# Performance work log

Hardware: AMD Instinct MI355X
Metric: run time of the kernel (lower is better)

Reference implementation:

```python
import jax, jax.numpy as jnp
import numpy as np
from jax import lax

B, S, T = 32, 400, 100
V, OOV = 32000, 100
E, U, AU, GP, ENC = 512, 256, 256, 256, 512


def setup_inputs() -> dict:
    key = jax.random.key(0)
    ks = jax.random.split(key, 24)
    r = lambda k, shp: 0.02 * jax.random.normal(k, shp, dtype=jnp.float32)
    inp = {
        "gt_tokens": jax.random.randint(ks[0], (B, T), 0, V, dtype=jnp.int32),
        "extended_input_tokens": jax.random.randint(ks[1], (B, S), 0, V + OOV, dtype=jnp.int32),
        "enc_output": jax.random.normal(ks[2], (B, S, ENC), dtype=jnp.float32),
        "enc_attn": jax.random.normal(ks[3], (B, S, AU), dtype=jnp.float32),
        "h0": jnp.zeros((B, U), jnp.float32),
        "c0": jnp.zeros((B, U), jnp.float32),
        # learned parameters
        "emb": r(ks[4], (V, E)),
        "lstm_kernel": r(ks[5], (E, 4 * U)),
        "lstm_rec": r(ks[6], (U, 4 * U)),
        "lstm_bias": jnp.zeros((4 * U,), jnp.float32),
        "attn_Wd": r(ks[7], (2 * U, AU)),
        "attn_bd": jnp.zeros((AU,), jnp.float32),
        "attn_Wc": r(ks[8], (1, AU)),
        "attn_Wa": r(ks[9], (AU, 1)),
        "clf_W1": r(ks[10], (U, U)),
        "clf_b1": jnp.zeros((U,), jnp.float32),
        "clf_W2": r(ks[11], (U, V)),
        "clf_b2": jnp.zeros((V,), jnp.float32),
        "gp_Ws": r(ks[12], (2 * U, GP)),
        "gp_Wc": r(ks[13], (ENC, GP)),
        "gp_Wi": r(ks[14], (E, GP)),
        "gp_bi": jnp.zeros((GP,), jnp.float32),
        "gp_Wg": r(ks[15], (GP, 1)),
    }
    return inp


def _decode(gt_tokens, extended_input_tokens, enc_output, enc_attn, h0, c0,
            emb, lstm_kernel, lstm_rec, lstm_bias, attn_Wd, attn_bd, attn_Wc,
            attn_Wa, clf_W1, clf_b1, clf_W2, clf_b2, gp_Ws, gp_Wc, gp_Wi,
            gp_bi, gp_Wg):
    Bn, Sn = extended_input_tokens.shape
    gt_vec = emb[gt_tokens]                      # [B,T,E] teacher-forced inputs
    xs = jnp.swapaxes(gt_vec, 0, 1)              # [T,B,E]
    batch_idx = jnp.arange(Bn)[:, None]

    def step(carry, x):
        h, c, cov = carry                        # [B,U],[B,U],[B,S]
        # single-step LSTM (TF gate order i,f,g,o)
        z = x @ lstm_kernel + h @ lstm_rec + lstm_bias
        i_, f_, g_, o_ = jnp.split(z, 4, axis=-1)
        c = jax.nn.sigmoid(f_) * c + jax.nn.sigmoid(i_) * jnp.tanh(g_)
        h = jax.nn.sigmoid(o_) * jnp.tanh(c)
        dec_state = jnp.concatenate([h, c], axis=1)          # [B,2U]
        # Bahdanau attention with coverage
        dec_attn = dec_state @ attn_Wd + attn_bd             # [B,AU]
        cov_attn = cov[:, :, None] * attn_Wc[0]              # [B,S,AU]
        scores = jnp.tanh(enc_attn + cov_attn + dec_attn[:, None, :]) @ attn_Wa
        a = jax.nn.softmax(scores, axis=1)[:, :, 0]          # [B,S]
        c_vec = jnp.einsum('bse,bs->be', enc_output, a)      # [B,ENC]
        cov_loss = jnp.sum(jnp.minimum(cov, a), axis=1)      # [B]
        cov = cov + a
        # pg: faithful scalar quirk ([0,0,0] of broadcast sum in original)
        g = dec_state[0] @ gp_Ws + c_vec[0] @ gp_Wc + (x[0] @ gp_Wi + gp_bi)
        pg = jax.nn.sigmoid((g @ gp_Wg)[0])
        # vocab distribution, extended with OOV zeros
        vocab_p = jax.nn.softmax((h @ clf_W1 + clf_b1) @ clf_W2 + clf_b2, axis=-1)
        vocab_p = jnp.concatenate([vocab_p, jnp.zeros((Bn, OOV), vocab_p.dtype)], axis=1)
        # copy distribution via scatter-add of attention onto extended ids
        sent_p = jnp.zeros((Bn, V + OOV), a.dtype).at[batch_idx, extended_input_tokens].add(a)
        final = pg * vocab_p + (1.0 - pg) * sent_p           # [B,V+OOV]
        tok = jnp.argmax(final, axis=1).astype(jnp.int32)
        return (h, c, cov), (final, tok, cov_loss)

    cov0 = jnp.zeros((Bn, Sn), jnp.float32)
    _, (probs, seqs, cov_losses) = lax.scan(step, (h0, c0, cov0), xs)
    return (jnp.swapaxes(probs, 0, 1),       # [B,T,V+OOV]
            jnp.swapaxes(seqs, 0, 1),        # [B,T]
            jnp.swapaxes(cov_losses, 0, 1))  # [B,T]


def reference(gt_tokens, extended_input_tokens, enc_output, enc_attn, h0, c0,
              emb, lstm_kernel, lstm_rec, lstm_bias, attn_Wd, attn_bd,
              attn_Wc, attn_Wa, clf_W1, clf_b1, clf_W2, clf_b2, gp_Ws, gp_Wc,
              gp_Wi, gp_bi, gp_Wg):
    return _decode(gt_tokens, extended_input_tokens, enc_output, enc_attn, h0,
                   c0, emb, lstm_kernel, lstm_rec, lstm_bias, attn_Wd,
                   attn_bd, attn_Wc, attn_Wa, clf_W1, clf_b1, clf_W2, clf_b2,
                   gp_Ws, gp_Wc, gp_Wi, gp_bi, gp_Wg)
```

## Files before the change

kernel.cpp:

```cpp
#include <hip/hip_runtime.h>
#include <hip/hip_bf16.h>

#define Bn 32
#define Sn 400
#define Tn 100
#define Vn 32000
#define OOVn 100
#define VEn 32100
#define En 512
#define Un 256
#define AUn 256
#define GPn 256
#define ENCn 512
#define Z4n 1024

typedef __attribute__((ext_vector_type(8))) short bf16x8;
typedef __attribute__((ext_vector_type(4))) float f32x4;
typedef unsigned short ushort_t;
typedef unsigned long long u64;

__device__ __forceinline__ float rcp_f(float x){ return __builtin_amdgcn_rcpf(x); }
__device__ __forceinline__ float tanh_fast(float x){
  float e2 = __expf(2.f*x);
  return 1.f - 2.f*rcp_f(e2 + 1.f);
}
__device__ __forceinline__ float sigmoid_f(float x){ return 1.f/(1.f+__expf(-x)); }
__device__ __forceinline__ ushort_t f2bf(float f){
  unsigned u = __float_as_uint(f);
  unsigned r = (u + 0x7FFFu + ((u>>16)&1u)) >> 16;
  return (ushort_t)r;
}
__device__ __forceinline__ u64 shfl_xor_u64(u64 v, int m){
  unsigned lo = (unsigned)v, hi = (unsigned)(v>>32);
  lo = (unsigned)__shfl_xor((int)lo, m);
  hi = (unsigned)__shfl_xor((int)hi, m);
  return ((u64)hi<<32)|(u64)lo;
}

__device__ __forceinline__ void st_rlx(float* p, float v){
  __hip_atomic_store(p, v, __ATOMIC_RELAXED, __HIP_MEMORY_SCOPE_AGENT);
}
__device__ __forceinline__ float ld_rlx(const float* p){
  return __hip_atomic_load(p, __ATOMIC_RELAXED, __HIP_MEMORY_SCOPE_AGENT);
}
__device__ __forceinline__ void st_flag(unsigned* p, unsigned v){
  __hip_atomic_store(p, v, __ATOMIC_RELAXED, __HIP_MEMORY_SCOPE_AGENT);
}
__device__ __forceinline__ unsigned ld_flag(const unsigned* p){
  return __hip_atomic_load(p, __ATOMIC_RELAXED, __HIP_MEMORY_SCOPE_AGENT);
}


__global__ __launch_bounds__(256) void k_zx(const int* __restrict__ gt,
    const float* __restrict__ emb, const float* __restrict__ Wk,
    const float* __restrict__ bias, float* __restrict__ Zx,
    unsigned* __restrict__ bars, float* __restrict__ covloss){
  __shared__ float As[64][17];
  __shared__ float Bs[16][65];
  __shared__ int tok_lds[64];
  int r0 = blockIdx.x * 64;
  int c0 = blockIdx.y * 64;
  int tid = threadIdx.x;
  int ty = tid >> 4, tx = tid & 15;
  if (blockIdx.x == 0){
    int y = blockIdx.y;
    #pragma unroll
    for (int i = 0; i < 2; ++i){
      int idx = y*512 + i*256 + tid;
      bars[idx] = 0u;
    }
    if (tid < 200) covloss[y*200 + tid] = 0.f;
  }
  if (tid < 64){
    int r = r0 + tid;
    tok_lds[tid] = gt[(r & 31)*Tn + (r >> 5)];
  }
  __syncthreads();
  float acc[4][4] = {};
  for (int k0 = 0; k0 < En; k0 += 16){
    #pragma unroll
    for (int p = 0; p < 4; ++p){
      int row = (tid>>4) + p*16, kk = tid & 15;
      As[row][kk] = emb[(size_t)tok_lds[row]*En + k0 + kk];
    }
    #pragma unroll
    for (int p = 0; p < 4; ++p){
      int kk = (tid>>6) + p*4, cc = tid & 63;
      Bs[kk][cc] = Wk[(size_t)(k0+kk)*Z4n + c0 + cc];
    }
    __syncthreads();
    #pragma unroll
    for (int kk = 0; kk < 16; ++kk){
      float av[4], bv[4];
      #pragma unroll
      for (int i=0;i<4;++i) av[i] = As[ty*4+i][kk];
      #pragma unroll
      for (int j=0;j<4;++j) bv[j] = Bs[kk][tx*4+j];
      #pragma unroll
      for (int i=0;i<4;++i)
        #pragma unroll
        for (int j=0;j<4;++j) acc[i][j] += av[i]*bv[j];
    }
    __syncthreads();
  }
  #pragma unroll
  for (int i=0;i<4;++i){
    int row = r0 + ty*4 + i;
    #pragma unroll
    for (int j=0;j<4;++j){
      int col = c0 + tx*4 + j;
      Zx[(size_t)row*Z4n + col] = acc[i][j] + bias[col];
    }
  }
}


__global__ __launch_bounds__(1024, 1) void k_loop(
    const float* __restrict__ Zx, const float* __restrict__ Wr,
    const float* __restrict__ Wd, const float* __restrict__ bd,
    const float* __restrict__ Wc, const float* __restrict__ Wa,
    const float* __restrict__ enc_attn,
    const float* __restrict__ h0, const float* __restrict__ c0,
    float* __restrict__ h_all, float* __restrict__ decp,
    float* __restrict__ c0_all, float* __restrict__ a_all,
    float* __restrict__ covloss, float* __restrict__ spart,
    unsigned* __restrict__ bars){
  __shared__ float Wr_lds[256*128];
  __shared__ float hfull[Un];
  __shared__ float ppart[8][132];
  __shared__ float zx_lds[128];
  __shared__ float zfull[128];
  __shared__ float hnew[32], cown[32];
  __shared__ float dec_lds[AUn];
  __shared__ float cov_lds[50], sc_lds[50];
  __shared__ float wred[16];
  __shared__ float red8[8];

  const int b = blockIdx.x & 31, k = blockIdx.x >> 5;
  const int tid = threadIdx.x, lane = tid & 63, w = tid >> 6;
  unsigned* flags = bars + b*8*32;
  unsigned* myflag = flags + k*32;

  for (int idx = tid; idx < 256*128; idx += 1024){
    int u = idx >> 7, jl = idx & 127;
    int gcol = 32*k + (jl & 31) + 256*(jl >> 5);
    Wr_lds[idx] = Wr[(size_t)u*Z4n + gcol];
  }
  if (tid < 32) cown[tid] = c0[b*Un + 32*k + tid];
  if (tid < 50) cov_lds[tid] = 0.f;
  const float4 wc4 = *(const float4*)(Wc + lane*4);
  const float4 wa4 = *(const float4*)(Wa + lane*4);
  if (tid < 256) hfull[tid] = h0[b*Un + tid];
  if (tid >= 256 && tid < 384){
    int jl = tid - 256;
    int gcol = 32*k + (jl & 31) + 256*(jl >> 5);
    zx_lds[jl] = Zx[(size_t)(0*Bn + b)*Z4n + gcol];
  }
  __syncthreads();

  {
    int p = tid >> 7, jl = tid & 127;
    float acc = 0.f;
    const float* wr = Wr_lds + (p*32)*128 + jl;
    const float* hb = hfull + p*32;
    #pragma unroll 8
    for (int uu = 0; uu < 32; ++uu) acc += hb[uu]*wr[uu*128];
    ppart[p][jl] = acc;
  }
  __syncthreads();
  if (tid < 128){
    float s = zx_lds[tid];
    #pragma unroll
    for (int q = 0; q < 8; ++q) s += ppart[q][tid];
    zfull[tid] = s;
  }
  __syncthreads();
  if (tid < 32){
    float zi = zfull[tid], zf = zfull[32+tid], zg = zfull[64+tid], zo = zfull[96+tid];
    float cn = sigmoid_f(zf)*cown[tid] + sigmoid_f(zi)*tanhf(zg);
    float hn = sigmoid_f(zo)*tanhf(cn);
    cown[tid] = cn; hnew[tid] = hn;
    int col = 32*k + tid;
    st_rlx(h_all + (size_t)(0*Bn + b)*Un + col, hn);
    if (b == 0) c0_all[0*Un + col] = cn;
  }
  __syncthreads();
  if (tid < 256){
    int c = tid;
    float acc = 0.f;
    const float* wdh = Wd + (size_t)(32*k)*AUn + c;
    #pragma unroll 8
    for (int u = 0; u < 32; ++u) acc += hnew[u]*wdh[(size_t)u*AUn];
    const float* wdc = Wd + (size_t)(Un + 32*k)*AUn + c;
    #pragma unroll 8
    for (int u = 0; u < 32; ++u) acc += cown[u]*wdc[(size_t)u*AUn];
    st_rlx(decp + (size_t)(b*8 + k)*256 + c, acc);
  }
  __syncthreads();
  if (tid == 0) st_flag(myflag, 1u);

  for (int t = 0; t < Tn; ++t){
    const int cur = t & 1, oth = cur ^ 1;
    if (tid < 8){
      while (ld_flag(flags + tid*32) < (unsigned)(t+1))
        __builtin_amdgcn_s_sleep(1);
    }
    __syncthreads();
    if (tid < 256){
      hfull[tid] = ld_rlx(h_all + (size_t)(t*Bn + b)*Un + tid);
    } else if (tid < 512){
      int c = tid - 256;
      float s = bd[c];
      const float* dp = decp + (size_t)cur*(Bn*8*256) + (size_t)(b*8)*256 + c;
      #pragma unroll
      for (int q = 0; q < 8; ++q) s += ld_rlx(dp + q*256);
      dec_lds[c] = s;
    } else if (tid < 520){
      red8[tid-512] = (t > 0) ? ld_rlx(spart + oth*(Bn*8) + b*8 + (tid-512)) : 0.f;
    } else if (tid >= 576 && tid < 704 && t + 1 < Tn){
      int jl = tid - 576;
      int gcol = 32*k + (jl & 31) + 256*(jl >> 5);
      zx_lds[jl] = Zx[(size_t)((t+1)*Bn + b)*Z4n + gcol];
    }
    __syncthreads();
    if (t > 0 && w == 0){
      float pv = (lane < 8) ? red8[lane] : 0.f;
      pv += __shfl_xor(pv, 1); pv += __shfl_xor(pv, 2); pv += __shfl_xor(pv, 4);
      float inv = 1.f / __shfl(pv, 0);
      float clp = 0.f;
      if (lane < 50){
        float aa = sc_lds[lane] * inv;
        float co = cov_lds[lane];
        a_all[(size_t)((t-1)*Bn + b)*Sn + 50*k + lane] = aa;
        clp = fminf(co, aa);
        cov_lds[lane] = co + aa;
      }
      #pragma unroll
      for (int m = 1; m < 64; m <<= 1) clp += __shfl_xor(clp, m);
      if (lane == 0) atomicAdd(&covloss[b*Tn + (t-1)], clp);
    }
    {
      int p = tid >> 7, jl = tid & 127;
      float acc = 0.f;
      const float* wr = Wr_lds + (p*32)*128 + jl;
      const float* hb = hfull + p*32;
      #pragma unroll 8
      for (int uu = 0; uu < 32; ++uu) acc += hb[uu]*wr[uu*128];
      ppart[p][jl] = acc;
    }
    __syncthreads();
    if (tid < 128 && t + 1 < Tn){
      float s = zx_lds[tid];
      #pragma unroll
      for (int q = 0; q < 8; ++q) s += ppart[q][tid];
      zfull[tid] = s;
    }
    __syncthreads();
    if (tid < 32 && t + 1 < Tn){
      float zi = zfull[tid], zf = zfull[32+tid], zg = zfull[64+tid], zo = zfull[96+tid];
      float cn = sigmoid_f(zf)*cown[tid] + sigmoid_f(zi)*tanhf(zg);
      float hn = sigmoid_f(zo)*tanhf(cn);
      cown[tid] = cn; hnew[tid] = hn;
      int col = 32*k + tid;
      st_rlx(h_all + (size_t)((t+1)*Bn + b)*Un + col, hn);
      if (b == 0) c0_all[(t+1)*Un + col] = cn;
    }
    __syncthreads();
    if (w < 4){
      if (t + 1 < Tn){
        int c = tid;
        float acc = 0.f;
        const float* wdh = Wd + (size_t)(32*k)*AUn + c;
        #pragma unroll 8
        for (int u = 0; u < 32; ++u) acc += hnew[u]*wdh[(size_t)u*AUn];
        const float* wdc = Wd + (size_t)(Un + 32*k)*AUn + c;
        #pragma unroll 8
        for (int u = 0; u < 32; ++u) acc += cown[u]*wdc[(size_t)u*AUn];
        st_rlx(decp + (size_t)oth*(Bn*8*256) + (size_t)(b*8 + k)*256 + c, acc);
      }
    } else {
      const float4 da = *(const float4*)(dec_lds + lane*4);
      float wsum = 0.f;
      for (int sl = w - 4; sl < 50; sl += 12){
        float cvv = cov_lds[sl];
        const float4 e = *(const float4*)(enc_attn + ((size_t)(b*Sn + 50*k + sl))*AUn + lane*4);
        float psc = tanh_fast(e.x + cvv*wc4.x + da.x)*wa4.x
                  + tanh_fast(e.y + cvv*wc4.y + da.y)*wa4.y
                  + tanh_fast(e.z + cvv*wc4.z + da.z)*wa4.z
                  + tanh_fast(e.w + cvv*wc4.w + da.w)*wa4.w;
        #pragma unroll
        for (int m = 1; m < 64; m <<= 1) psc += __shfl_xor(psc, m);
        if (lane == 0){
          float ev = __expf(psc);
          sc_lds[sl] = ev;
          wsum += ev;
        }
      }
      if (lane == 0) wred[w] = wsum;
    }
    __syncthreads();
    if (tid == 0){
      float S = 0.f;
      #pragma unroll
      for (int q = 4; q < 16; ++q) S += wred[q];
      st_rlx(spart + cur*(Bn*8) + b*8 + k, S);
    }
    __syncthreads();
    if (tid == 0) st_flag(myflag, (unsigned)(t + 2));
  }

  if (tid < 8){
    while (ld_flag(flags + tid*32) < (unsigned)(Tn + 1))
      __builtin_amdgcn_s_sleep(1);
  }
  __syncthreads();
  if (tid < 8) red8[tid] = ld_rlx(spart + ((Tn-1)&1)*(Bn*8) + b*8 + tid);
  __syncthreads();
  if (w == 0){
    float pv = (lane < 8) ? red8[lane] : 0.f;
    pv += __shfl_xor(pv, 1); pv += __shfl_xor(pv, 2); pv += __shfl_xor(pv, 4);
    float inv = 1.f / __shfl(pv, 0);
    float clp = 0.f;
    if (lane < 50){
      float aa = sc_lds[lane] * inv;
      float co = cov_lds[lane];
      a_all[(size_t)((Tn-1)*Bn + b)*Sn + 50*k + lane] = aa;
      clp = fminf(co, aa);
    }
    #pragma unroll
    for (int m = 1; m < 64; m <<= 1) clp += __shfl_xor(clp, m);
    if (lane == 0) atomicAdd(&covloss[b*Tn + (Tn-1)], clp);
  }
}


__global__ __launch_bounds__(256) void k_misc(
    const float* __restrict__ W2, ushort_t* __restrict__ W2T,
    const float* __restrict__ h_all, const float* __restrict__ W1,
    const float* __restrict__ b1, ushort_t* __restrict__ hid,
    const int* __restrict__ gt, const float* __restrict__ emb,
    const float* __restrict__ gpWi, const float* __restrict__ gpbi,
    const float* __restrict__ a_all, const float* __restrict__ enc_out,
    const float* __restrict__ c0_all, const float* __restrict__ gpWs,
    const float* __restrict__ gpWc, const float* __restrict__ gpWg,
    float* __restrict__ pg, float* __restrict__ Ssum, u64* __restrict__ amax){
  __shared__ __align__(16) char sbuf[32768];
  int bid = blockIdx.x, tid = threadIdx.x;
  if (bid < 2000){
    if (bid < 13){
      int idx = bid*256 + tid;
      if (idx < 3200) Ssum[idx] = 0.f;
    } else if (bid < 26){
      int idx = (bid-13)*256 + tid;
      if (idx < 3200) amax[idx] = 0ull;
    }
    float (*tile)[65] = (float(*)[65])sbuf;
    int n0 = (bid % 500) * 64, k0 = (bid / 500) * 64;
    int tx = tid & 63, ty4 = tid >> 6;
    #pragma unroll
    for (int i = 0; i < 16; ++i){
      int kk = ty4 + i*4;
      tile[kk][tx] = W2[(size_t)(k0+kk)*Vn + n0 + tx];
    }
    __syncthreads();
    #pragma unroll
    for (int i = 0; i < 16; ++i){
      int n = ty4 + i*4;
      W2T[(size_t)(n0+n)*Un + k0 + tx] = f2bf(tile[tx][n]);
    }
  } else if (bid < 2100){
    float* hl = (float*)sbuf;
    int t = bid - 2000;
    for (int i = tid; i < Bn*Un; i += 256) hl[i] = h_all[(size_t)t*Bn*Un + i];
    __syncthreads();
    int j = tid;
    float bj = b1[j];
    float acc[32];
    #pragma unroll
    for (int r = 0; r < 32; ++r) acc[r] = bj;
    for (int u = 0; u < Un; ++u){
      float wv = W1[u*Un + j];
      #pragma unroll
      for (int r = 0; r < 32; ++r) acc[r] += hl[r*Un + u]*wv;
    }
    #pragma unroll
    for (int r = 0; r < 32; ++r) hid[(size_t)(t*Bn + r)*Un + j] = f2bf(acc[r]);
  } else {
    int t = bid - 2100;
    float* al  = (float*)sbuf;
    float* cv  = al + 400;
    float* xl  = cv + 512;
    float* red = xl + 512;
    for (int s = tid; s < Sn; s += 256) al[s] = a_all[(size_t)(t*Bn)*Sn + s];
    for (int i = tid; i < En; i += 256) xl[i] = emb[(size_t)gt[t]*En + i];
    __syncthreads();
    for (int e = tid; e < ENCn; e += 256){
      float acc = 0.f;
      for (int s = 0; s < Sn; ++s) acc += enc_out[(size_t)s*ENCn + e]*al[s];
      cv[e] = acc;
    }
    __syncthreads();
    int j = tid;
    float g = gpbi[j];
    for (int u = 0; u < En; ++u) g += xl[u]*gpWi[u*GPn + j];
    const float* h0r = h_all + (size_t)t*Bn*Un;
    const float* c0r = c0_all + t*Un;
    for (int u = 0; u < Un; ++u) g += h0r[u]*gpWs[u*GPn + j];
    for (int u = 0; u < Un; ++u) g += c0r[u]*gpWs[(Un+u)*GPn + j];
    for (int e = 0; e < ENCn; ++e) g += cv[e]*gpWc[e*GPn + j];
    float v = g * gpWg[j];
    int lane = tid & 63, wv2 = tid >> 6;
    #pragma unroll
    for (int m = 1; m < 64; m <<= 1) v += __shfl_xor(v, m);
    if (lane == 0) red[wv2] = v;
    __syncthreads();
    if (tid == 0) pg[t] = 1.f/(1.f+__expf(-(red[0]+red[1]+red[2]+red[3])));
  }
}

__global__ __launch_bounds__(512, 1) void k_gemm(const ushort_t* __restrict__ A,
    const ushort_t* __restrict__ Bw, const float* __restrict__ b2,
    float* __restrict__ Ssum, u64* __restrict__ amax, const float* __restrict__ pg,
    float* __restrict__ probs, int mode){
  __shared__ ushort_t Bs[256*264];
  int gx = blockIdx.x;
  int n0 = blockIdx.y * 256;
  int tid = threadIdx.x;
  int lane = tid & 63, w = tid >> 6;
  {
    int rr = tid >> 1, half = (tid & 1) * 128;
    const ushort_t* gb = Bw + (size_t)(n0 + rr)*Un + half;
    ushort_t* lb = Bs + rr*264 + half;
    #pragma unroll
    for (int j = 0; j < 16; ++j)
      *((uint4*)lb + j) = *((const uint4*)gb + j);
  }
  __syncthreads();

  int cbase = (gx == 0) ? 0 : 13;
  int nch   = (gx == 0) ? 13 : 12;
  float bb[4];
  for (int ci = 0; ci < nch; ++ci){
    int r0 = (cbase + ci) * 128;
    bf16x8 af[8];
    {
      const ushort_t* ar = A + (size_t)(r0 + w*16 + (lane&15))*Un + (lane>>4)*8;
      #pragma unroll
      for (int kk = 0; kk < 8; ++kk) af[kk] = *(const bf16x8*)(ar + kk*32);
    }
    f32x4 acc[16];
    #pragma unroll
    for (int i = 0; i < 16; ++i) acc[i] = (f32x4){0.f,0.f,0.f,0.f};
    #pragma unroll
    for (int kk = 0; kk < 8; ++kk){
      #pragma unroll
      for (int nt = 0; nt < 16; ++nt){
        bf16x8 bf = *(const bf16x8*)(Bs + (nt*16 + (lane&15))*264 + kk*32 + (lane>>4)*8);
        acc[nt] = __builtin_amdgcn_mfma_f32_16x16x32_bf16(af[kk], bf, acc[nt], 0, 0, 0);
      }
    }
    int rowloc = w*16 + (lane>>4)*4;
    if (mode == 0){
      float rs[4] = {0.f,0.f,0.f,0.f};
      #pragma unroll
      for (int nt = 0; nt < 16; ++nt){
        int v = n0 + nt*16 + (lane&15);
        float b2v = b2[v];
        #pragma unroll
        for (int i = 0; i < 4; ++i) rs[i] += __expf(acc[nt][i] + b2v);
      }
      #pragma unroll
      for (int m = 1; m < 16; m <<= 1)
        #pragma unroll
        for (int i = 0; i < 4; ++i) rs[i] += __shfl_xor(rs[i], m);
      if ((lane&15) == 0)
        #pragma unroll
        for (int i = 0; i < 4; ++i) atomicAdd(&Ssum[r0+rowloc+i], rs[i]);
    } else {
      float sc[4]; size_t obase[4];
      #pragma unroll
      for (int i = 0; i < 4; ++i){
        int r = r0+rowloc+i; int tt = r>>5, bbx = r&31;
        sc[i] = pg[tt] / Ssum[r];
        obase[i] = (size_t)(bbx*Tn+tt)*VEn;
      }
      u64 pm[4] = {0,0,0,0};
      #pragma unroll
      for (int nt = 0; nt < 16; ++nt){
        int v = n0 + nt*16 + (lane&15);
        float b2v = b2[v];
        #pragma unroll
        for (int i = 0; i < 4; ++i){
          float val = __expf(acc[nt][i] + b2v) * sc[i];
          __builtin_nontemporal_store(val, &probs[obase[i] + v]);
          u64 p = ((u64)__float_as_uint(val)<<32) | (u64)(0xFFFFFFFFu - (unsigned)v);
          pm[i] = p > pm[i] ? p : pm[i];
        }
      }
      #pragma unroll
      for (int m = 1; m < 16; m <<= 1)
        #pragma unroll
        for (int i = 0; i < 4; ++i){
          u64 o = shfl_xor_u64(pm[i], m);
          pm[i] = o > pm[i] ? o : pm[i];
        }
      if ((lane&15) == 0)
        #pragma unroll
        for (int i = 0; i < 4; ++i) atomicMax(&amax[r0+rowloc+i], pm[i]);
    }
  }
  (void)bb;
}

__global__ __launch_bounds__(256) void k_scatter(const int* __restrict__ ext,
    const float* __restrict__ a_all, const float* __restrict__ pg,
    float* __restrict__ probs, const u64* __restrict__ amax,
    float* __restrict__ seqs){
  __shared__ int   hkey[1024];
  __shared__ float hval[1024];
  __shared__ u64   wmax[4];
  int r = blockIdx.x; int t = r>>5, b = r&31;
  float c1 = 1.f - pg[t];
  int tid = threadIdx.x;
  #pragma unroll
  for (int i = 0; i < 4; ++i){
    hkey[tid + i*256] = -1;
    hval[tid + i*256] = 0.f;
  }
  size_t obase = (size_t)(b*Tn + t)*VEn;
  if (tid < OOVn) probs[obase + Vn + tid] = 0.f;
  __syncthreads();
  for (int s = tid; s < Sn; s += 256){
    int key = ext[b*Sn + s];
    float v = c1 * a_all[(size_t)r*Sn + s];
    unsigned h = ((unsigned)key * 2654435761u) >> 22;
    for (;;){
      int old = atomicCAS(&hkey[h], -1, key);
      if (old == -1 || old == key) break;
      h = (h + 1) & 1023;
    }
    atomicAdd(&hval[h], v);
  }
  __syncthreads();
  u64 pm = 0;
  #pragma unroll
  for (int i = 0; i < 4; ++i){
    int slot = tid + i*256;
    int tk = hkey[slot];
    if (tk >= 0){
      float nv = probs[obase + tk] + hval[slot];
      probs[obase + tk] = nv;
      u64 p = ((u64)__float_as_uint(nv)<<32) | (u64)(0xFFFFFFFFu - (unsigned)tk);
      pm = p > pm ? p : pm;
    }
  }
  #pragma unroll
  for (int m = 1; m < 64; m <<= 1){
    u64 o = shfl_xor_u64(pm, m);
    pm = o > pm ? o : pm;
  }
  int lane = tid & 63, w = tid >> 6;
  if (lane == 0) wmax[w] = pm;
  __syncthreads();
  if (tid == 0){
    u64 mm = amax[r];
    #pragma unroll
    for (int q = 0; q < 4; ++q) mm = wmax[q] > mm ? wmax[q] : mm;
    unsigned tk = 0xFFFFFFFFu - (unsigned)(mm & 0xFFFFFFFFull);
    seqs[b*Tn + t] = (float)tk;
  }
}


extern "C" void kernel_launch(void* const* d_in, const int* in_sizes, int n_in,
                              void* d_out, int out_size, void* d_ws, size_t ws_size,
                              hipStream_t stream){
  (void)in_sizes; (void)n_in; (void)out_size; (void)ws_size;
  const int*   gt       = (const int*)d_in[0];
  const int*   ext      = (const int*)d_in[1];
  const float* enc_out  = (const float*)d_in[2];
  const float* enc_attn = (const float*)d_in[3];
  const float* h0       = (const float*)d_in[4];
  const float* c0       = (const float*)d_in[5];
  const float* emb      = (const float*)d_in[6];
  const float* Wk       = (const float*)d_in[7];
  const float* Wr       = (const float*)d_in[8];
  const float* lb       = (const float*)d_in[9];
  const float* Wd       = (const float*)d_in[10];
  const float* bd       = (const float*)d_in[11];
  const float* Wc       = (const float*)d_in[12];
  const float* Wa       = (const float*)d_in[13];
  const float* W1       = (const float*)d_in[14];
  const float* b1       = (const float*)d_in[15];
  const float* W2       = (const float*)d_in[16];
  const float* b2       = (const float*)d_in[17];
  const float* gpWs     = (const float*)d_in[18];
  const float* gpWc     = (const float*)d_in[19];
  const float* gpWi     = (const float*)d_in[20];
  const float* gpbi     = (const float*)d_in[21];
  const float* gpWg     = (const float*)d_in[22];

  float* probs   = (float*)d_out;
  float* seqs    = probs + (size_t)Bn*Tn*VEn;
  float* covloss = seqs + Bn*Tn;

  char* wp = (char*)d_ws;
  auto carve = [&](size_t bytes)->void*{
    void* p = (void*)wp; wp += (bytes + 255) & ~(size_t)255; return p;
  };
  float*    Zx      = (float*)carve((size_t)3200*Z4n*4);
  float*    h_all   = (float*)carve((size_t)Tn*Bn*Un*4);
  float*    decp    = (float*)carve((size_t)2*Bn*8*256*4);
  float*    c0_all  = (float*)carve((size_t)Tn*Un*4);
  float*    a_all   = (float*)carve((size_t)3200*Sn*4);
  ushort_t* hid_bf  = (ushort_t*)carve((size_t)3200*Un*2);
  ushort_t* W2T     = (ushort_t*)carve((size_t)Vn*Un*2);
  float*    Ssum    = (float*)carve((size_t)3200*4);
  u64*      amax    = (u64*)carve((size_t)3200*8);
  float*    pg      = (float*)carve((size_t)Tn*4);
  float*    spart   = (float*)carve((size_t)2*Bn*8*4);
  unsigned* bars    = (unsigned*)carve((size_t)Bn*8*32*4);

  k_zx  <<<dim3(50,16), 256, 0, stream>>>(gt, emb, Wk, lb, Zx, bars, covloss);

  k_loop<<<256, 1024, 0, stream>>>(Zx, Wr, Wd, bd, Wc, Wa, enc_attn,
                                   h0, c0, h_all, decp, c0_all,
                                   a_all, covloss, spart, bars);

  k_misc<<<2200, 256, 0, stream>>>(W2, W2T, h_all, W1, b1, hid_bf,
                                   gt, emb, gpWi, gpbi, a_all, enc_out,
                                   c0_all, gpWs, gpWc, gpWg, pg, Ssum, amax);
  k_gemm<<<dim3(2,125), 512, 0, stream>>>(hid_bf, W2T, b2, Ssum, amax, pg, probs, 0);
  k_gemm<<<dim3(2,125), 512, 0, stream>>>(hid_bf, W2T, b2, Ssum, amax, pg, probs, 1);
  k_scatter<<<3200, 256, 0, stream>>>(ext, a_all, pg, probs, amax, seqs);
}
```

Before: 1.182 ms.

## Fuse post-loop kernels into one persistent kernel with grid flag barriers

Moves the W2 transpose/bf16 conversion into the Zx precompute kernel. Merges the hidden projection, pointer-gen gate, the two vocab GEMM passes and the scatter into a single persistent 250-block kernel that synchronises through global flag barriers. Per-slice partial sums and argmax results are now written to buffers and reduced deterministically rather than with atomics. This removes several launch gaps and tail effects. In exchange it adds spin-wait barriers that need every block to be co-resident, and it puts the small prologue work on a subset of the blocks.

```diff
diff --git a/kernel.cpp b/kernel.cpp
--- a/kernel.cpp
+++ b/kernel.cpp
@@ -13,6 +13,7 @@
 #define GPn 256
 #define ENCn 512
 #define Z4n 1024
+#define NPB 250
 
 typedef __attribute__((ext_vector_type(8))) short bf16x8;
 typedef __attribute__((ext_vector_type(4))) float f32x4;
@@ -43,6 +44,15 @@
 __device__ __forceinline__ float ld_rlx(const float* p){
   return __hip_atomic_load(p, __ATOMIC_RELAXED, __HIP_MEMORY_SCOPE_AGENT);
 }
+__device__ __forceinline__ void st_rlxu(unsigned* p, unsigned v){
+  __hip_atomic_store(p, v, __ATOMIC_RELAXED, __HIP_MEMORY_SCOPE_AGENT);
+}
+__device__ __forceinline__ void st_rlx64(u64* p, u64 v){
+  __hip_atomic_store(p, v, __ATOMIC_RELAXED, __HIP_MEMORY_SCOPE_AGENT);
+}
+__device__ __forceinline__ u64 ld_rlx64(const u64* p){
+  return __hip_atomic_load(p, __ATOMIC_RELAXED, __HIP_MEMORY_SCOPE_AGENT);
+}
 __device__ __forceinline__ void st_flag(unsigned* p, unsigned v){
   __hip_atomic_store(p, v, __ATOMIC_RELAXED, __HIP_MEMORY_SCOPE_AGENT);
 }
@@ -54,20 +64,24 @@
 __global__ __launch_bounds__(256) void k_zx(const int* __restrict__ gt,
     const float* __restrict__ emb, const float* __restrict__ Wk,
     const float* __restrict__ bias, float* __restrict__ Zx,
-    unsigned* __restrict__ bars, float* __restrict__ covloss){
-  __shared__ float As[64][17];
-  __shared__ float Bs[16][65];
-  __shared__ int tok_lds[64];
+    const float* __restrict__ W2, ushort_t* __restrict__ W2T,
+    unsigned* __restrict__ bars, unsigned* __restrict__ bars2,
+    float* __restrict__ covloss){
+  __shared__ __align__(16) char zbuf[16640];
+  float (*As)[17] = (float(*)[17])zbuf;
+  float (*Bs)[65] = (float(*)[65])(zbuf + 4352);
+  int*   tok_lds  = (int*)(zbuf + 4352 + 4160);
   int r0 = blockIdx.x * 64;
   int c0 = blockIdx.y * 64;
   int tid = threadIdx.x;
-  int ty = tid >> 4, tx = tid & 15;
+  int ty = tid >> 4, tx16 = tid & 15;
   if (blockIdx.x == 0){
     int y = blockIdx.y;
     #pragma unroll
     for (int i = 0; i < 2; ++i){
       int idx = y*512 + i*256 + tid;
       bars[idx] = 0u;
+      if (idx < NPB*32) bars2[idx] = 0u;
     }
     if (tid < 200) covloss[y*200 + tid] = 0.f;
   }
@@ -95,7 +109,7 @@
       #pragma unroll
       for (int i=0;i<4;++i) av[i] = As[ty*4+i][kk];
       #pragma unroll
-      for (int j=0;j<4;++j) bv[j] = Bs[kk][tx*4+j];
+      for (int j=0;j<4;++j) bv[j] = Bs[kk][tx16*4+j];
       #pragma unroll
       for (int i=0;i<4;++i)
         #pragma unroll
@@ -108,8 +122,28 @@
     int row = r0 + ty*4 + i;
     #pragma unroll
     for (int j=0;j<4;++j){
-      int col = c0 + tx*4 + j;
+      int col = c0 + tx16*4 + j;
       Zx[(size_t)row*Z4n + col] = acc[i][j] + bias[col];
+    }
+  }
+  float (*tl)[65] = (float(*)[65])zbuf;
+  int tx = tid & 63, ty4 = tid >> 6;
+  int bid = blockIdx.x*16 + blockIdx.y;
+  for (int rep = 0; rep < 3; ++rep){
+    int tile = bid + rep*800;
+    if (tile >= 2000) break;
+    int n0 = (tile % 500) * 64, k0 = (tile / 500) * 64;
+    __syncthreads();
+    #pragma unroll
+    for (int i = 0; i < 16; ++i){
+      int kk = ty4 + i*4;
+      tl[kk][tx] = W2[(size_t)(k0+kk)*Vn + n0 + tx];
+    }
+    __syncthreads();
+    #pragma unroll
+    for (int i = 0; i < 16; ++i){
+      int n = ty4 + i*4;
+      W2T[(size_t)(n0+n)*Un + k0 + tx] = f2bf(tl[tx][n]);
     }
   }
 }
@@ -334,8 +368,7 @@
 }
 
 
-__global__ __launch_bounds__(256) void k_misc(
-    const float* __restrict__ W2, ushort_t* __restrict__ W2T,
+__global__ __launch_bounds__(512, 1) void k_post(
     const float* __restrict__ h_all, const float* __restrict__ W1,
     const float* __restrict__ b1, ushort_t* __restrict__ hid,
     const int* __restrict__ gt, const float* __restrict__ emb,
@@ -343,108 +376,99 @@
     const float* __restrict__ a_all, const float* __restrict__ enc_out,
     const float* __restrict__ c0_all, const float* __restrict__ gpWs,
     const float* __restrict__ gpWc, const float* __restrict__ gpWg,
-    float* __restrict__ pg, float* __restrict__ Ssum, u64* __restrict__ amax){
-  __shared__ __align__(16) char sbuf[32768];
-  int bid = blockIdx.x, tid = threadIdx.x;
-  if (bid < 2000){
-    if (bid < 13){
-      int idx = bid*256 + tid;
-      if (idx < 3200) Ssum[idx] = 0.f;
-    } else if (bid < 26){
-      int idx = (bid-13)*256 + tid;
-      if (idx < 3200) amax[idx] = 0ull;
-    }
-    float (*tile)[65] = (float(*)[65])sbuf;
-    int n0 = (bid % 500) * 64, k0 = (bid / 500) * 64;
-    int tx = tid & 63, ty4 = tid >> 6;
-    #pragma unroll
-    for (int i = 0; i < 16; ++i){
-      int kk = ty4 + i*4;
-      tile[kk][tx] = W2[(size_t)(k0+kk)*Vn + n0 + tx];
-    }
-    __syncthreads();
-    #pragma unroll
-    for (int i = 0; i < 16; ++i){
-      int n = ty4 + i*4;
-      W2T[(size_t)(n0+n)*Un + k0 + tx] = f2bf(tile[tx][n]);
-    }
-  } else if (bid < 2100){
-    float* hl = (float*)sbuf;
-    int t = bid - 2000;
-    for (int i = tid; i < Bn*Un; i += 256) hl[i] = h_all[(size_t)t*Bn*Un + i];
-    __syncthreads();
-    int j = tid;
+    float* __restrict__ pg, const ushort_t* __restrict__ W2T,
+    const float* __restrict__ b2, float* __restrict__ Sp,
+    float* __restrict__ Ssum, u64* __restrict__ Ap,
+    float* __restrict__ probs, const int* __restrict__ ext,
+    float* __restrict__ seqs, unsigned* __restrict__ bars2){
+  __shared__ __align__(16) char sb[135168];
+  __shared__ u64 wmax8[8];
+  __shared__ float red4[4];
+  const int gid = blockIdx.x, tid = threadIdx.x;
+  const int lane = tid & 63, w = tid >> 6;
+  unsigned* myflag = bars2 + gid*32;
+
+  if (gid < 100){
+    int t = gid;
+    float* hl = (float*)sb;
+    for (int i = tid; i < Bn*Un; i += 512) hl[i] = h_all[(size_t)t*Bn*Un + i];
+    __syncthreads();
+    int j = tid & 255, p = tid >> 8;
     float bj = b1[j];
-    float acc[32];
-    #pragma unroll
-    for (int r = 0; r < 32; ++r) acc[r] = bj;
+    float acc[16];
+    #pragma unroll
+    for (int i = 0; i < 16; ++i) acc[i] = bj;
     for (int u = 0; u < Un; ++u){
       float wv = W1[u*Un + j];
-      #pragma unroll
-      for (int r = 0; r < 32; ++r) acc[r] += hl[r*Un + u]*wv;
-    }
-    #pragma unroll
-    for (int r = 0; r < 32; ++r) hid[(size_t)(t*Bn + r)*Un + j] = f2bf(acc[r]);
-  } else {
-    int t = bid - 2100;
-    float* al  = (float*)sbuf;
-    float* cv  = al + 400;
-    float* xl  = cv + 512;
-    float* red = xl + 512;
-    for (int s = tid; s < Sn; s += 256) al[s] = a_all[(size_t)(t*Bn)*Sn + s];
-    for (int i = tid; i < En; i += 256) xl[i] = emb[(size_t)gt[t]*En + i];
-    __syncthreads();
-    for (int e = tid; e < ENCn; e += 256){
+      const float* hp = hl + (p*16)*Un + u;
+      #pragma unroll
+      for (int i = 0; i < 16; ++i) acc[i] += hp[i*Un] * wv;
+    }
+    __syncthreads();
+    ushort_t* hidL = (ushort_t*)sb;
+    #pragma unroll
+    for (int i = 0; i < 16; ++i) hidL[(p*16+i)*Un + j] = f2bf(acc[i]);
+    __syncthreads();
+    unsigned* hw = (unsigned*)hid + (size_t)t*4096;
+    const unsigned* hs = (const unsigned*)hidL;
+    for (int i = tid; i < 4096; i += 512) st_rlxu(hw + i, hs[i]);
+  } else if (gid < 200){
+    int t = gid - 100;
+    float* al = (float*)sb;
+    float* cv = al + 400;
+    float* xl = cv + 512;
+    for (int s = tid; s < Sn; s += 512) al[s] = a_all[(size_t)(t*Bn)*Sn + s];
+    for (int i = tid; i < En; i += 512) xl[i] = emb[(size_t)gt[t]*En + i];
+    __syncthreads();
+    if (tid < ENCn){
       float acc = 0.f;
-      for (int s = 0; s < Sn; ++s) acc += enc_out[(size_t)s*ENCn + e]*al[s];
-      cv[e] = acc;
-    }
-    __syncthreads();
-    int j = tid;
-    float g = gpbi[j];
-    for (int u = 0; u < En; ++u) g += xl[u]*gpWi[u*GPn + j];
-    const float* h0r = h_all + (size_t)t*Bn*Un;
-    const float* c0r = c0_all + t*Un;
-    for (int u = 0; u < Un; ++u) g += h0r[u]*gpWs[u*GPn + j];
-    for (int u = 0; u < Un; ++u) g += c0r[u]*gpWs[(Un+u)*GPn + j];
-    for (int e = 0; e < ENCn; ++e) g += cv[e]*gpWc[e*GPn + j];
-    float v = g * gpWg[j];
-    int lane = tid & 63, wv2 = tid >> 6;
-    #pragma unroll
-    for (int m = 1; m < 64; m <<= 1) v += __shfl_xor(v, m);
-    if (lane == 0) red[wv2] = v;
-    __syncthreads();
-    if (tid == 0) pg[t] = 1.f/(1.f+__expf(-(red[0]+red[1]+red[2]+red[3])));
-  }
-}
-
-__global__ __launch_bounds__(512, 1) void k_gemm(const ushort_t* __restrict__ A,
-    const ushort_t* __restrict__ Bw, const float* __restrict__ b2,
-    float* __restrict__ Ssum, u64* __restrict__ amax, const float* __restrict__ pg,
-    float* __restrict__ probs, int mode){
-  __shared__ ushort_t Bs[256*264];
-  int gx = blockIdx.x;
-  int n0 = blockIdx.y * 256;
-  int tid = threadIdx.x;
-  int lane = tid & 63, w = tid >> 6;
+      for (int s = 0; s < Sn; ++s) acc += enc_out[(size_t)s*ENCn + tid]*al[s];
+      cv[tid] = acc;
+    }
+    __syncthreads();
+    if (tid < 256){
+      int j = tid;
+      float g = gpbi[j];
+      for (int u = 0; u < En; ++u) g += xl[u]*gpWi[u*GPn + j];
+      const float* h0r = h_all + (size_t)t*Bn*Un;
+      const float* c0r = c0_all + t*Un;
+      for (int u = 0; u < Un; ++u) g += h0r[u]*gpWs[u*GPn + j];
+      for (int u = 0; u < Un; ++u) g += c0r[u]*gpWs[(Un+u)*GPn + j];
+      for (int e = 0; e < ENCn; ++e) g += cv[e]*gpWc[e*GPn + j];
+      float v = g * gpWg[j];
+      #pragma unroll
+      for (int m = 1; m < 64; m <<= 1) v += __shfl_xor(v, m);
+      if (lane == 0) red4[w] = v;
+    }
+    __syncthreads();
+    if (tid == 0)
+      st_rlx(&pg[t], 1.f/(1.f+__expf(-(red4[0]+red4[1]+red4[2]+red4[3]))));
+  }
+  __syncthreads();
+  if (tid == 0) st_flag(myflag, 1u);
+  if (tid < NPB){ while (ld_flag(bars2 + tid*32) < 1u) __builtin_amdgcn_s_sleep(1); }
+  __syncthreads();
+
+  ushort_t* Bs = (ushort_t*)sb;
+  const int slice = gid % 125, gx = gid / 125;
+  const int n0 = slice * 256;
   {
     int rr = tid >> 1, half = (tid & 1) * 128;
-    const ushort_t* gb = Bw + (size_t)(n0 + rr)*Un + half;
+    const ushort_t* gb = W2T + (size_t)(n0 + rr)*Un + half;
     ushort_t* lb = Bs + rr*264 + half;
     #pragma unroll
-    for (int j = 0; j < 16; ++j)
-      *((uint4*)lb + j) = *((const uint4*)gb + j);
-  }
-  __syncthreads();
-
-  int cbase = (gx == 0) ? 0 : 13;
-  int nch   = (gx == 0) ? 13 : 12;
-  float bb[4];
+    for (int j2 = 0; j2 < 16; ++j2)
+      *((uint4*)lb + j2) = *((const uint4*)gb + j2);
+  }
+  __syncthreads();
+  const int cbase = gx ? 13 : 0;
+  const int nch   = gx ? 12 : 13;
+
   for (int ci = 0; ci < nch; ++ci){
     int r0 = (cbase + ci) * 128;
     bf16x8 af[8];
     {
-      const ushort_t* ar = A + (size_t)(r0 + w*16 + (lane&15))*Un + (lane>>4)*8;
+      const ushort_t* ar = hid + (size_t)(r0 + w*16 + (lane&15))*Un + (lane>>4)*8;
       #pragma unroll
       for (int kk = 0; kk < 8; ++kk) af[kk] = *(const bf16x8*)(ar + kk*32);
     }
@@ -459,115 +483,155 @@
         acc[nt] = __builtin_amdgcn_mfma_f32_16x16x32_bf16(af[kk], bf, acc[nt], 0, 0, 0);
       }
     }
+    float rs[4] = {0.f,0.f,0.f,0.f};
+    #pragma unroll
+    for (int nt = 0; nt < 16; ++nt){
+      int v = n0 + nt*16 + (lane&15);
+      float b2v = b2[v];
+      #pragma unroll
+      for (int i = 0; i < 4; ++i) rs[i] += __expf(acc[nt][i] + b2v);
+    }
+    #pragma unroll
+    for (int m = 1; m < 16; m <<= 1)
+      #pragma unroll
+      for (int i = 0; i < 4; ++i) rs[i] += __shfl_xor(rs[i], m);
+    if ((lane&15) == 0){
+      int rowloc = w*16 + (lane>>4)*4;
+      #pragma unroll
+      for (int i = 0; i < 4; ++i)
+        st_rlx(&Sp[(size_t)slice*3200 + r0 + rowloc + i], rs[i]);
+    }
+  }
+  __syncthreads();
+  if (tid == 0) st_flag(myflag, 2u);
+  if (tid < NPB){ while (ld_flag(bars2 + tid*32) < 2u) __builtin_amdgcn_s_sleep(1); }
+  __syncthreads();
+
+  if (gid < 7){
+    int r = gid*512 + tid;
+    if (r < 3200){
+      float s = 0.f;
+      for (int sl = 0; sl < 125; ++sl) s += ld_rlx(&Sp[(size_t)sl*3200 + r]);
+      st_rlx(&Ssum[r], s);
+    }
+  }
+  __syncthreads();
+  if (tid == 0) st_flag(myflag, 3u);
+  if (tid < NPB){ while (ld_flag(bars2 + tid*32) < 3u) __builtin_amdgcn_s_sleep(1); }
+  __syncthreads();
+
+  for (int ci = 0; ci < nch; ++ci){
+    int r0 = (cbase + ci) * 128;
+    bf16x8 af[8];
+    {
+      const ushort_t* ar = hid + (size_t)(r0 + w*16 + (lane&15))*Un + (lane>>4)*8;
+      #pragma unroll
+      for (int kk = 0; kk < 8; ++kk) af[kk] = *(const bf16x8*)(ar + kk*32);
+    }
+    f32x4 acc[16];
+    #pragma unroll
+    for (int i = 0; i < 16; ++i) acc[i] = (f32x4){0.f,0.f,0.f,0.f};
+    #pragma unroll
+    for (int kk = 0; kk < 8; ++kk){
+      #pragma unroll
+      for (int nt = 0; nt < 16; ++nt){
+        bf16x8 bf = *(const bf16x8*)(Bs + (nt*16 + (lane&15))*264 + kk*32 + (lane>>4)*8);
+        acc[nt] = __builtin_amdgcn_mfma_f32_16x16x32_bf16(af[kk], bf, acc[nt], 0, 0, 0);
+      }
+    }
     int rowloc = w*16 + (lane>>4)*4;
-    if (mode == 0){
-      float rs[4] = {0.f,0.f,0.f,0.f};
-      #pragma unroll
-      for (int nt = 0; nt < 16; ++nt){
-        int v = n0 + nt*16 + (lane&15);
-        float b2v = b2[v];
-        #pragma unroll
-        for (int i = 0; i < 4; ++i) rs[i] += __expf(acc[nt][i] + b2v);
-      }
-      #pragma unroll
-      for (int m = 1; m < 16; m <<= 1)
-        #pragma unroll
-        for (int i = 0; i < 4; ++i) rs[i] += __shfl_xor(rs[i], m);
-      if ((lane&15) == 0)
-        #pragma unroll
-        for (int i = 0; i < 4; ++i) atomicAdd(&Ssum[r0+rowloc+i], rs[i]);
-    } else {
-      float sc[4]; size_t obase[4];
+    float sc[4]; size_t obase[4];
+    #pragma unroll
+    for (int i = 0; i < 4; ++i){
+      int r = r0 + rowloc + i; int tt = r>>5, bb = r&31;
+      sc[i] = ld_rlx(&pg[tt]) / Ssum[r];
+      obase[i] = (size_t)(bb*Tn + tt)*VEn;
+    }
+    u64 pm[4] = {0,0,0,0};
+    #pragma unroll
+    for (int nt = 0; nt < 16; ++nt){
+      int v = n0 + nt*16 + (lane&15);
+      float b2v = b2[v];
       #pragma unroll
       for (int i = 0; i < 4; ++i){
-        int r = r0+rowloc+i; int tt = r>>5, bbx = r&31;
-        sc[i] = pg[tt] / Ssum[r];
-        obase[i] = (size_t)(bbx*Tn+tt)*VEn;
-      }
-      u64 pm[4] = {0,0,0,0};
-      #pragma unroll
-      for (int nt = 0; nt < 16; ++nt){
-        int v = n0 + nt*16 + (lane&15);
-        float b2v = b2[v];
-        #pragma unroll
-        for (int i = 0; i < 4; ++i){
-          float val = __expf(acc[nt][i] + b2v) * sc[i];
-          __builtin_nontemporal_store(val, &probs[obase[i] + v]);
-          u64 p = ((u64)__float_as_uint(val)<<32) | (u64)(0xFFFFFFFFu - (unsigned)v);
-          pm[i] = p > pm[i] ? p : pm[i];
-        }
-      }
-      #pragma unroll
-      for (int m = 1; m < 16; m <<= 1)
-        #pragma unroll
-        for (int i = 0; i < 4; ++i){
-          u64 o = shfl_xor_u64(pm[i], m);
-          pm[i] = o > pm[i] ? o : pm[i];
-        }
-      if ((lane&15) == 0)
-        #pragma unroll
-        for (int i = 0; i < 4; ++i) atomicMax(&amax[r0+rowloc+i], pm[i]);
-    }
-  }
-  (void)bb;
-}
-
-__global__ __launch_bounds__(256) void k_scatter(const int* __restrict__ ext,
-    const float* __restrict__ a_all, const float* __restrict__ pg,
-    float* __restrict__ probs, const u64* __restrict__ amax,
-    float* __restrict__ seqs){
-  __shared__ int   hkey[1024];
-  __shared__ float hval[1024];
-  __shared__ u64   wmax[4];
-  int r = blockIdx.x; int t = r>>5, b = r&31;
-  float c1 = 1.f - pg[t];
-  int tid = threadIdx.x;
-  #pragma unroll
-  for (int i = 0; i < 4; ++i){
-    hkey[tid + i*256] = -1;
-    hval[tid + i*256] = 0.f;
-  }
-  size_t obase = (size_t)(b*Tn + t)*VEn;
-  if (tid < OOVn) probs[obase + Vn + tid] = 0.f;
-  __syncthreads();
-  for (int s = tid; s < Sn; s += 256){
-    int key = ext[b*Sn + s];
-    float v = c1 * a_all[(size_t)r*Sn + s];
-    unsigned h = ((unsigned)key * 2654435761u) >> 22;
-    for (;;){
-      int old = atomicCAS(&hkey[h], -1, key);
-      if (old == -1 || old == key) break;
-      h = (h + 1) & 1023;
-    }
-    atomicAdd(&hval[h], v);
-  }
-  __syncthreads();
-  u64 pm = 0;
-  #pragma unroll
-  for (int i = 0; i < 4; ++i){
-    int slot = tid + i*256;
-    int tk = hkey[slot];
-    if (tk >= 0){
-      float nv = probs[obase + tk] + hval[slot];
-      probs[obase + tk] = nv;
-      u64 p = ((u64)__float_as_uint(nv)<<32) | (u64)(0xFFFFFFFFu - (unsigned)tk);
-      pm = p > pm ? p : pm;
-    }
-  }
-  #pragma unroll
-  for (int m = 1; m < 64; m <<= 1){
-    u64 o = shfl_xor_u64(pm, m);
-    pm = o > pm ? o : pm;
-  }
-  int lane = tid & 63, w = tid >> 6;
-  if (lane == 0) wmax[w] = pm;
-  __syncthreads();
-  if (tid == 0){
-    u64 mm = amax[r];
-    #pragma unroll
-    for (int q = 0; q < 4; ++q) mm = wmax[q] > mm ? wmax[q] : mm;
-    unsigned tk = 0xFFFFFFFFu - (unsigned)(mm & 0xFFFFFFFFull);
-    seqs[b*Tn + t] = (float)tk;
+        float val = __expf(acc[nt][i] + b2v) * sc[i];
+        __builtin_nontemporal_store(val, &probs[obase[i] + v]);
+        u64 p = ((u64)__float_as_uint(val)<<32) | (u64)(0xFFFFFFFFu - (unsigned)v);
+        pm[i] = p > pm[i] ? p : pm[i];
+      }
+    }
+    #pragma unroll
+    for (int m = 1; m < 16; m <<= 1)
+      #pragma unroll
+      for (int i = 0; i < 4; ++i){
+        u64 o = shfl_xor_u64(pm[i], m);
+        pm[i] = o > pm[i] ? o : pm[i];
+      }
+    if ((lane&15) == 0)
+      #pragma unroll
+      for (int i = 0; i < 4; ++i)
+        st_rlx64(&Ap[(size_t)slice*3200 + r0 + rowloc + i], pm[i]);
+  }
+  __syncthreads();
+  if (tid == 0) st_flag(myflag, 4u);
+  if (tid < NPB){ while (ld_flag(bars2 + tid*32) < 4u) __builtin_amdgcn_s_sleep(1); }
+  __syncthreads();
+
+  int* hkey = (int*)sb;
+  float* hval = (float*)(sb + 4096);
+  for (int rep = 0; rep < 13; ++rep){
+    int r = rep*250 + gid;
+    if (r >= 3200) break;
+    int t = r >> 5, b = r & 31;
+    #pragma unroll
+    for (int i = 0; i < 2; ++i){
+      hkey[tid + i*512] = -1;
+      hval[tid + i*512] = 0.f;
+    }
+    size_t obase = (size_t)(b*Tn + t)*VEn;
+    if (tid < OOVn) probs[obase + Vn + tid] = 0.f;
+    u64 vm = (tid < 125) ? ld_rlx64(&Ap[(size_t)tid*3200 + r]) : 0ull;
+    float c1 = 1.f - ld_rlx(&pg[t]);
+    __syncthreads();
+    if (tid < Sn){
+      int key = ext[b*Sn + tid];
+      float v = c1 * a_all[(size_t)r*Sn + tid];
+      unsigned h = ((unsigned)key * 2654435761u) >> 22;
+      for (;;){
+        int old = atomicCAS(&hkey[h], -1, key);
+        if (old == -1 || old == key) break;
+        h = (h + 1) & 1023;
+      }
+      atomicAdd(&hval[h], v);
+    }
+    __syncthreads();
+    u64 pm = vm;
+    #pragma unroll
+    for (int i = 0; i < 2; ++i){
+      int slot = tid + i*512;
+      int tk = hkey[slot];
+      if (tk >= 0){
+        float nv = probs[obase + tk] + hval[slot];
+        probs[obase + tk] = nv;
+        u64 p = ((u64)__float_as_uint(nv)<<32) | (u64)(0xFFFFFFFFu - (unsigned)tk);
+        pm = p > pm ? p : pm;
+      }
+    }
+    #pragma unroll
+    for (int m = 1; m < 64; m <<= 1){
+      u64 o = shfl_xor_u64(pm, m);
+      pm = o > pm ? o : pm;
+    }
+    if (lane == 0) wmax8[w] = pm;
+    __syncthreads();
+    if (tid == 0){
+      u64 mm = wmax8[0];
+      #pragma unroll
+      for (int q = 1; q < 8; ++q) mm = wmax8[q] > mm ? wmax8[q] : mm;
+      unsigned tk = 0xFFFFFFFFu - (unsigned)(mm & 0xFFFFFFFFull);
+      seqs[b*Tn + t] = (float)tk;
+    }
+    __syncthreads();
   }
 }
 
@@ -616,21 +680,22 @@
   ushort_t* hid_bf  = (ushort_t*)carve((size_t)3200*Un*2);
   ushort_t* W2T     = (ushort_t*)carve((size_t)Vn*Un*2);
   float*    Ssum    = (float*)carve((size_t)3200*4);
-  u64*      amax    = (u64*)carve((size_t)3200*8);
+  float*    Sp      = (float*)carve((size_t)125*3200*4);
+  u64*      Ap      = (u64*)carve((size_t)125*3200*8);
   float*    pg      = (float*)carve((size_t)Tn*4);
   float*    spart   = (float*)carve((size_t)2*Bn*8*4);
   unsigned* bars    = (unsigned*)carve((size_t)Bn*8*32*4);
-
-  k_zx  <<<dim3(50,16), 256, 0, stream>>>(gt, emb, Wk, lb, Zx, bars, covloss);
+  unsigned* bars2   = (unsigned*)carve((size_t)NPB*32*4);
+
+  k_zx  <<<dim3(50,16), 256, 0, stream>>>(gt, emb, Wk, lb, Zx, W2, W2T,
+                                          bars, bars2, covloss);
 
   k_loop<<<256, 1024, 0, stream>>>(Zx, Wr, Wd, bd, Wc, Wa, enc_attn,
                                    h0, c0, h_all, decp, c0_all,
                                    a_all, covloss, spart, bars);
 
-  k_misc<<<2200, 256, 0, stream>>>(W2, W2T, h_all, W1, b1, hid_bf,
-                                   gt, emb, gpWi, gpbi, a_all, enc_out,
-                                   c0_all, gpWs, gpWc, gpWg, pg, Ssum, amax);
-  k_gemm<<<dim3(2,125), 512, 0, stream>>>(hid_bf, W2T, b2, Ssum, amax, pg, probs, 0);
-  k_gemm<<<dim3(2,125), 512, 0, stream>>>(hid_bf, W2T, b2, Ssum, amax, pg, probs, 1);
-  k_scatter<<<3200, 256, 0, stream>>>(ext, a_all, pg, probs, amax, seqs);
-}
+  k_post<<<NPB, 512, 0, stream>>>(h_all, W1, b1, hid_bf, gt, emb,
+                                  gpWi, gpbi, a_all, enc_out, c0_all,
+                                  gpWs, gpWc, gpWg, pg, W2T, b2,
+                                  Sp, Ssum, Ap, probs, ext, seqs, bars2);
+}
```

Measured after the change: 1.144 ms. 1.03x faster.
